# Kernel tuning notes

Measured on AMD Instinct MI355X. Metric: run time of the kernel, lower is better.

## Reference

```python
import jax, jax.numpy as jnp
import numpy as np

B, T, D = 4, 8192, 512
E, F, CAP = 8, 2048, 4096


def setup_inputs() -> dict:
    key = jax.random.key(0)
    ks = jax.random.split(key, 6)
    s = 0.02
    return {
        "x": jax.random.normal(ks[0], (B, T, D), dtype=jnp.float32),
        "Wr": jax.random.normal(ks[1], (D, E), dtype=jnp.float32) * s,
        "W1": jax.random.normal(ks[2], (E, D, F), dtype=jnp.float32) * s,
        "b1": jax.random.normal(ks[3], (E, F), dtype=jnp.float32) * s,
        "W2": jax.random.normal(ks[4], (E, F, D), dtype=jnp.float32) * s,
        "b2": jax.random.normal(ks[5], (E, D), dtype=jnp.float32) * s,
    }


def reference(x, Wr, W1, b1, W2, b2):
    Bb, Tt, Dd = x.shape
    N = Bb * Tt
    C = min(CAP, N)
    x_flat = x.reshape(N, Dd)
    logits = x_flat @ Wr                      # [N, E]
    probs = jax.nn.softmax(logits, axis=0)    # softmax over tokens (dim=0)
    # per-expert top-C tokens
    vals, idx = jax.lax.top_k(probs.T, C)     # [E, C]
    selected = x_flat[idx]                    # [E, C, D] gather
    h = jax.nn.gelu(jnp.einsum('ecd,edf->ecf', selected, W1) + b1[:, None, :],
                    approximate=False)
    out_e = jnp.einsum('ecf,efd->ecd', h, W2) + b2[:, None, :]  # [E, C, D]
    weighted = vals[..., None] * out_e
    output = jnp.zeros_like(x_flat).at[idx.reshape(-1)].add(weighted.reshape(-1, Dd))
    return output.reshape(Bb, Tt, Dd)
```

## Files before the change

kernel.cpp:

```cpp
#include <hip/hip_runtime.h>
#include <math.h>

#define N_TOK 32768
#define DIM 512
#define NE 8
#define NF 2048
#define CCAP 4096

typedef __attribute__((ext_vector_type(4))) float floatx4;
typedef __attribute__((ext_vector_type(8))) short shortx8;
typedef __attribute__((ext_vector_type(4))) short shortx4;

__device__ __forceinline__ short f2bf(float f) {
  union { float f; unsigned u; } v; v.f = f;
  unsigned r = v.u + 0x7FFFu + ((v.u >> 16) & 1u);
  return (short)(r >> 16);
}

__device__ __forceinline__ float bf2f(short s) {
  union { unsigned u; float f; } v; v.u = ((unsigned)(unsigned short)s) << 16;
  return v.f;
}

__device__ __forceinline__ unsigned f2key(float f) {
  union { float f; unsigned u; } v; v.f = f;
  return (v.u & 0x80000000u) ? ~v.u : (v.u | 0x80000000u);
}

__device__ __forceinline__ void gll16(const void* g, void* l) {
  __builtin_amdgcn_global_load_lds(
      (const __attribute__((address_space(1))) void*)g,
      (__attribute__((address_space(3))) void*)l, 16, 0, 0);
}

__device__ __forceinline__ float fast_gelu(float h) {
  float u = 0.7978845608f * (h + 0.044715f * h * h * h);
  float au = fabsf(u) * 2.885390082f;
  float z = __builtin_amdgcn_exp2f(au);
  float th = 1.0f - 2.0f * __builtin_amdgcn_rcpf(1.0f + z);
  th = copysignf(th, u);
  return 0.5f * h * (1.0f + th);
}

__device__ __forceinline__ void stage8_adv(const short** ap, short* dst, int t) {
#pragma unroll
  for (int i = 0; i < 8; i++) gll16(ap[i], dst + i * 2048 + t * 8);
#pragma unroll
  for (int i = 0; i < 8; i++) ap[i] += 64;
}

__device__ __forceinline__ void stage8_g2(const short* gA, short* dst, int t, int kk) {
#pragma unroll
  for (int i = 0; i < 8; i++)
    gll16(gA + (size_t)i * 32 * NF + kk * 64, dst + i * 2048 + t * 8);
}

__device__ __forceinline__ void loadB(const short* gB, int koff, int ldb, shortx8* bf) {
#pragma unroll
  for (int g = 0; g < 2; g++)
#pragma unroll
    for (int j = 0; j < 4; j++)
      bf[g * 4 + j] = *(const shortx8*)(gB + (size_t)j * 16 * ldb + koff + g * 32);
}

__device__ __forceinline__ void compute64r(const short* ldsA, const shortx8* bf,
                                           floatx4 (*acc)[4], int arow, int lx, int q) {
#pragma unroll
  for (int g = 0; g < 2; g++) {
    const int pu = (((g << 2) | q) ^ lx) << 3;
#pragma unroll
    for (int i = 0; i < 8; i++) {
      shortx8 af = *(const shortx8*)&ldsA[(arow + i * 16) * 64 + pu];
#pragma unroll
      for (int j = 0; j < 4; j++)
        acc[i][j] = __builtin_amdgcn_mfma_f32_16x16x32_bf16(af, bf[g * 4 + j], acc[i][j], 0, 0, 0);
    }
  }
}

__device__ __forceinline__ void xcd_map(int& bx, int& by, int& zi) {
  int lid = blockIdx.x + gridDim.x * (blockIdx.y + gridDim.y * blockIdx.z);
  int k = 8 / (int)gridDim.z;
  int x = lid & 7, rem = lid >> 3;
  zi = x / k;
  int bxy = rem * k + (x % k);
  bx = bxy % (int)gridDim.x;
  by = bxy / (int)gridDim.x;
}

__global__ __launch_bounds__(256) void k_prep(
    const float* __restrict__ x, const float* __restrict__ W1,
    const float* __restrict__ W2, const float* __restrict__ Wr,
    float* __restrict__ out, short* __restrict__ xb,
    short* __restrict__ w1t, short* __restrict__ w2t,
    float* __restrict__ logitsT, int* __restrict__ cnt) {
  __shared__ float tl[64 * 68];
  const int b = blockIdx.x, t = threadIdx.x;
  if (b < 4096) {
    const float* in;
    short* o;
    int R, C, c0, r0;
    if (b < 2048) {
      int e = b >> 8, tlid = b & 255;
      in = W1 + (size_t)e * DIM * NF;
      o = w1t + (size_t)e * NF * DIM;
      R = DIM; C = NF;
      c0 = (tlid & 31) * 64; r0 = (tlid >> 5) * 64;
    } else {
      int bb = b - 2048;
      int e = bb >> 8, tlid = bb & 255;
      in = W2 + (size_t)e * NF * DIM;
      o = w2t + (size_t)e * DIM * NF;
      R = NF; C = DIM;
      c0 = (tlid & 7) * 64; r0 = (tlid >> 3) * 64;
    }
    const int r = t >> 4, cq = (t & 15) * 4;
#pragma unroll
    for (int ii = 0; ii < 4; ii++) {
      floatx4 v = *(const floatx4*)&in[(size_t)(r0 + r + 16 * ii) * C + c0 + cq];
      *(floatx4*)&tl[(r + 16 * ii) * 68 + cq] = v;
    }
    __syncthreads();
    const int cc = t >> 2, rq = (t & 3) * 16;
    shortx8 o0, o1;
#pragma unroll
    for (int k = 0; k < 8; k++) o0[k] = f2bf(tl[(rq + k) * 68 + cc]);
#pragma unroll
    for (int k = 0; k < 8; k++) o1[k] = f2bf(tl[(rq + 8 + k) * 68 + cc]);
    size_t ob = (size_t)(c0 + cc) * R + r0 + rq;
    *(shortx8*)&o[ob] = o0;
    *(shortx8*)&o[ob + 8] = o1;
  } else if (b < 4608) {
    const int base = (b - 4096) * 8192 + t;
    floatx4 z = {0.f, 0.f, 0.f, 0.f};
#pragma unroll
    for (int i = 0; i < 32; i++) *(floatx4*)&out[(size_t)(base + i * 256) * 4] = z;
  } else if (b < 5120) {
    const int base = (b - 4608) * 8192 + t;
#pragma unroll
    for (int i = 0; i < 32; i++) {
      floatx4 v = *(const floatx4*)&x[(size_t)(base + i * 256) * 4];
      shortx4 s;
      s.x = f2bf(v.x); s.y = f2bf(v.y); s.z = f2bf(v.z); s.w = f2bf(v.w);
      *(shortx4*)&xb[(size_t)(base + i * 256) * 4] = s;
    }
  } else if (b < 6144) {
    const int lane = t & 63;
    const int wave = (b - 5120) * 4 + (t >> 6);
    float wr[64];
#pragma unroll
    for (int i = 0; i < 16; i++)
      *(floatx4*)&wr[i * 4] = *(const floatx4*)&Wr[lane * 64 + i * 4];
    for (int n = wave; n < N_TOK; n += 4096) {
      const float* xr = x + (size_t)n * DIM + lane * 8;
      floatx4 x0 = *(const floatx4*)xr;
      floatx4 x1 = *(const floatx4*)(xr + 4);
      float xs[8] = {x0.x, x0.y, x0.z, x0.w, x1.x, x1.y, x1.z, x1.w};
      double acc[8];
#pragma unroll
      for (int e2 = 0; e2 < 8; e2++) acc[e2] = 0.0;
#pragma unroll
      for (int j = 0; j < 8; j++) {
        double xv = (double)xs[j];
#pragma unroll
        for (int e2 = 0; e2 < 8; e2++) acc[e2] += xv * (double)wr[j * 8 + e2];
      }
#pragma unroll
      for (int e2 = 0; e2 < 8; e2++) {
#pragma unroll
        for (int off2 = 32; off2 > 0; off2 >>= 1)
          acc[e2] += __shfl_xor(acc[e2], off2);
      }
      double rv = acc[0];
#pragma unroll
      for (int e2 = 1; e2 < 8; e2++)
        if (lane == e2) rv = acc[e2];
      if (lane < 8) logitsT[(size_t)lane * N_TOK + n] = (float)rv;
    }
  } else {
#pragma unroll
    for (int i = 0; i < 128; i++) cnt[t + 256 * i] = 0;
  }
}

__global__ __launch_bounds__(1024) void k_select(const float* __restrict__ logitsT,
                                                 int* __restrict__ sel_idx,
                                                 float* __restrict__ sel_val,
                                                 int* __restrict__ cnt,
                                                 int* __restrict__ slots) {
  __shared__ float redf[16];
  __shared__ unsigned redu[16];
  __shared__ float s_max, s_inv;
  __shared__ unsigned s_tot;
  __shared__ unsigned s_cnt[2];
  const int e = blockIdx.x, t = threadIdx.x;
  const int wid = t >> 6, lane = t & 63;
  const float* lg = logitsT + (size_t)e * N_TOK;
  float lv[32];
  unsigned kv[32];
#pragma unroll
  for (int i = 0; i < 32; i++) lv[i] = lg[i * 1024 + t];
#pragma unroll
  for (int i = 0; i < 32; i++) kv[i] = f2key(lv[i]);
  float m = lv[0];
#pragma unroll
  for (int i = 1; i < 32; i++) m = fmaxf(m, lv[i]);
#pragma unroll
  for (int o = 32; o > 0; o >>= 1) m = fmaxf(m, __shfl_xor(m, o));
  if (lane == 0) redf[wid] = m;
  __syncthreads();
  if (t == 0) {
    float v = redf[0];
    for (int i = 1; i < 16; i++) v = fmaxf(v, redf[i]);
    s_max = v;
  }
  __syncthreads();
  m = s_max;
  float s = 0.f;
#pragma unroll
  for (int i = 0; i < 32; i++) s += expf(lv[i] - m);
#pragma unroll
  for (int o = 32; o > 0; o >>= 1) s += __shfl_xor(s, o);
  if (lane == 0) redf[wid] = s;
  __syncthreads();
  if (t == 0) {
    float v = 0.f;
    for (int i = 0; i < 16; i++) v += redf[i];
    s_inv = 1.0f / v;
  }
  unsigned T = 0;
  for (int bb = 31; bb >= 0; --bb) {
    unsigned cand = T | (1u << bb);
    unsigned c = 0;
#pragma unroll
    for (int i = 0; i < 32; i++) c += (kv[i] >= cand) ? 1u : 0u;
#pragma unroll
    for (int o = 32; o > 0; o >>= 1) c += __shfl_xor(c, o);
    if (lane == 0) redu[wid] = c;
    __syncthreads();
    if (t == 0) {
      unsigned v = 0;
      for (int i = 0; i < 16; i++) v += redu[i];
      s_tot = v;
    }
    __syncthreads();
    if (s_tot >= CCAP) T = cand;
  }
  {
    unsigned c = 0;
#pragma unroll
    for (int i = 0; i < 32; i++) c += (kv[i] > T) ? 1u : 0u;
#pragma unroll
    for (int o = 32; o > 0; o >>= 1) c += __shfl_xor(c, o);
    if (lane == 0) redu[wid] = c;
    __syncthreads();
    if (t == 0) {
      unsigned v = 0;
      for (int i = 0; i < 16; i++) v += redu[i];
      s_tot = v;
      s_cnt[0] = 0;
      s_cnt[1] = 0;
    }
    __syncthreads();
  }
  const unsigned rr = CCAP - s_tot;
  const float inv = s_inv;
  const unsigned long long lmask = (1ull << lane) - 1ull;
#pragma unroll
  for (int i = 0; i < 32; i++) {
    int n = i * 1024 + t;
    bool gt = kv[i] > T;
    bool eq = kv[i] == T;
    unsigned long long mg = __ballot(gt);
    unsigned long long mq = __ballot(eq);
    unsigned bg = 0, bq = 0;
    if (lane == 0) {
      if (mg) bg = atomicAdd(&s_cnt[0], (unsigned)__popcll(mg));
      if (mq) bq = atomicAdd(&s_cnt[1], (unsigned)__popcll(mq));
    }
    bg = __shfl(bg, 0);
    bq = __shfl(bq, 0);
    int pos = -1;
    if (gt) {
      pos = (int)(bg + (unsigned)__popcll(mg & lmask));
    } else if (eq) {
      unsigned qq = bq + (unsigned)__popcll(mq & lmask);
      if (qq < rr) pos = (int)(CCAP - rr + qq);
    }
    if (pos >= 0) {
      sel_idx[e * CCAP + pos] = n;
      sel_val[e * CCAP + pos] = expf(lv[i] - m) * inv;
      int s2 = atomicAdd(&cnt[n], 1);
      slots[n * 8 + s2] = (e << 16) | pos;
    }
  }
}

__global__ __launch_bounds__(256, 2) void k_gemm1(
    const short* __restrict__ xb, const short* __restrict__ w1t,
    const float* __restrict__ b1, const int* __restrict__ sel_idx,
    short* __restrict__ H, int e0) {
  __shared__ char smem[256 * 136 * 2];
  short* ldsA0 = (short*)smem;
  short* ldsA1 = (short*)(smem + 32768);

  int bx, by, zi;
  xcd_map(bx, by, zi);
  const int e = e0 + zi;
  const int c0 = by * 256;
  const int f0 = bx * 128;
  const int t = threadIdx.x;
  const int lane = t & 63;
  const int w = t >> 6;
  const int wm = w & 1, wn = w >> 1;
  const int row8 = t >> 3;
  const int su = (t & 7) ^ (row8 & 7);

  const short* gAp[8];
#pragma unroll
  for (int i = 0; i < 8; i++) {
    int tok = sel_idx[e * CCAP + c0 + row8 + i * 32];
    gAp[i] = xb + (size_t)tok * DIM + su * 8;
  }
  const short* gB = w1t + ((size_t)(e * NF + f0 + wn * 64 + (lane & 15))) * DIM + (lane >> 4) * 8;

  floatx4 acc[8][4];
#pragma unroll
  for (int i = 0; i < 8; i++)
#pragma unroll
    for (int j = 0; j < 4; j++) acc[i][j] = (floatx4){0.f, 0.f, 0.f, 0.f};

  const int arow = wm * 128 + (lane & 15);
  const int lx = lane & 7, q = lane >> 4;

  stage8_adv(gAp, ldsA0, t);
  __syncthreads();

  for (int kk = 0; kk < DIM / 64; kk += 2) {
    {
      shortx8 bf[8];
      loadB(gB, kk * 64, DIM, bf);
      __builtin_amdgcn_sched_barrier(0);
      stage8_adv(gAp, ldsA1, t);
      __builtin_amdgcn_sched_barrier(0);
      compute64r(ldsA0, bf, acc, arow, lx, q);
      __syncthreads();
    }
    {
      shortx8 bf[8];
      loadB(gB, (kk + 1) * 64, DIM, bf);
      __builtin_amdgcn_sched_barrier(0);
      if (kk + 2 < DIM / 64) stage8_adv(gAp, ldsA0, t);
      __builtin_amdgcn_sched_barrier(0);
      compute64r(ldsA1, bf, acc, arow, lx, q);
      __syncthreads();
    }
  }

  short* ep = (short*)smem;
  const int colL = wn * 64 + (lane & 15);
  const int rowL = wm * 128 + ((lane >> 4) << 2);
#pragma unroll
  for (int j = 0; j < 4; j++) {
    float bv = b1[e * NF + f0 + colL + j * 16];
#pragma unroll
    for (int i = 0; i < 8; i++) {
#pragma unroll
      for (int r = 0; r < 4; r++) {
        float h = acc[i][j][r] + bv;
        ep[(rowL + i * 16 + r) * 136 + colL + j * 16] = f2bf(fast_gelu(h));
      }
    }
  }
  __syncthreads();
  short* Hp = H + (size_t)zi * CCAP * NF;
  const int chunk = t & 15;
#pragma unroll
  for (int it = 0; it < 16; it++) {
    int r = (t >> 4) + 16 * it;
    shortx8 v = *(const shortx8*)&ep[r * 136 + chunk * 8];
    *(shortx8*)&Hp[(size_t)(c0 + r) * NF + f0 + chunk * 8] = v;
  }
}

__global__ __launch_bounds__(256, 2) void k_gemm2(
    const short* __restrict__ H, const short* __restrict__ w2t,
    const float* __restrict__ b2, short* __restrict__ oute, int e0) {
  __shared__ char smem[256 * 136 * 2];
  short* ldsA0 = (short*)smem;
  short* ldsA1 = (short*)(smem + 32768);

  int bx, by, zi;
  xcd_map(bx, by, zi);
  const int e = e0 + zi;
  const int c0 = by * 256;
  const int d0 = bx * 128;
  const int t = threadIdx.x;
  const int lane = t & 63;
  const int w = t >> 6;
  const int wm = w & 1, wn = w >> 1;
  const int row8 = t >> 3;
  const int su = (t & 7) ^ (row8 & 7);

  const short* gA = H + ((size_t)zi * CCAP + c0 + row8) * NF + su * 8;
  const short* gB = w2t + ((size_t)(e * DIM + d0 + wn * 64 + (lane & 15))) * NF + (lane >> 4) * 8;

  floatx4 acc[8][4];
#pragma unroll
  for (int i = 0; i < 8; i++)
#pragma unroll
    for (int j = 0; j < 4; j++) acc[i][j] = (floatx4){0.f, 0.f, 0.f, 0.f};

  const int arow = wm * 128 + (lane & 15);
  const int lx = lane & 7, q = lane >> 4;

  stage8_g2(gA, ldsA0, t, 0);
  __syncthreads();

  for (int kk = 0; kk < NF / 64; kk += 2) {
    {
      shortx8 bf[8];
      loadB(gB, kk * 64, NF, bf);
      __builtin_amdgcn_sched_barrier(0);
      stage8_g2(gA, ldsA1, t, kk + 1);
      __builtin_amdgcn_sched_barrier(0);
      compute64r(ldsA0, bf, acc, arow, lx, q);
      __syncthreads();
    }
    {
      shortx8 bf[8];
      loadB(gB, (kk + 1) * 64, NF, bf);
      __builtin_amdgcn_sched_barrier(0);
      if (kk + 2 < NF / 64) stage8_g2(gA, ldsA0, t, kk + 2);
      __builtin_amdgcn_sched_barrier(0);
      compute64r(ldsA1, bf, acc, arow, lx, q);
      __syncthreads();
    }
  }

  short* ep = (short*)smem;
  const int colL = wn * 64 + (lane & 15);
  const int rowL = wm * 128 + ((lane >> 4) << 2);
#pragma unroll
  for (int j = 0; j < 4; j++) {
    float bv = b2[e * DIM + d0 + colL + j * 16];
#pragma unroll
    for (int i = 0; i < 8; i++) {
#pragma unroll
      for (int r = 0; r < 4; r++) {
        float o = acc[i][j][r] + bv;
        ep[(rowL + i * 16 + r) * 136 + colL + j * 16] = f2bf(o);
      }
    }
  }
  __syncthreads();
  const int chunk = t & 15;
#pragma unroll
  for (int it = 0; it < 16; it++) {
    int r = (t >> 4) + 16 * it;
    shortx8 v = *(const shortx8*)&ep[r * 136 + chunk * 8];
    *(shortx8*)&oute[((size_t)e * CCAP + c0 + r) * DIM + d0 + chunk * 8] = v;
  }
}

__global__ __launch_bounds__(256) void k_combine(
    const short* __restrict__ oute, const int* __restrict__ cnt,
    const int* __restrict__ slots, const float* __restrict__ sel_val,
    float* __restrict__ out) {
  const int lane = threadIdx.x & 63;
  const int wid = threadIdx.x >> 6;
  const int n = blockIdx.x * 4 + wid;
  const int c = cnt[n];
  if (c == 0) return;
  float acc[8];
#pragma unroll
  for (int k = 0; k < 8; k++) acc[k] = 0.f;
  for (int s = 0; s < c; ++s) {
    int sl = slots[n * 8 + s];
    int e = sl >> 16, pos = sl & 0xFFFF;
    float val = sel_val[e * CCAP + pos];
    shortx8 v = *(const shortx8*)&oute[((size_t)e * CCAP + pos) * DIM + lane * 8];
#pragma unroll
    for (int k = 0; k < 8; k++) acc[k] += val * bf2f(v[k]);
  }
  floatx4 o0 = {acc[0], acc[1], acc[2], acc[3]};
  floatx4 o1 = {acc[4], acc[5], acc[6], acc[7]};
  *(floatx4*)&out[(size_t)n * DIM + lane * 8] = o0;
  *(floatx4*)&out[(size_t)n * DIM + lane * 8 + 4] = o1;
}

extern "C" void kernel_launch(void* const* d_in, const int* in_sizes, int n_in,
                              void* d_out, int out_size, void* d_ws, size_t ws_size,
                              hipStream_t stream) {
  const float* x = (const float*)d_in[0];
  const float* Wr = (const float*)d_in[1];
  const float* W1 = (const float*)d_in[2];
  const float* b1 = (const float*)d_in[3];
  const float* W2 = (const float*)d_in[4];
  const float* b2 = (const float*)d_in[5];
  float* out = (float*)d_out;

  char* p = (char*)d_ws;
  size_t off = 0;
  auto carve = [&](size_t bytes) {
    void* r = p + off;
    off = (off + bytes + 255) & ~(size_t)255;
    return r;
  };
  short* xb = (short*)carve((size_t)N_TOK * DIM * 2);
  short* w1t = (short*)carve((size_t)NE * NF * DIM * 2);
  short* w2t = (short*)carve((size_t)NE * DIM * NF * 2);
  float* logitsT = (float*)carve((size_t)NE * N_TOK * 4);
  int* selidx = (int*)carve((size_t)NE * CCAP * 4);
  float* selval = (float*)carve((size_t)NE * CCAP * 4);
  int* cnt = (int*)carve((size_t)N_TOK * 4);
  int* slots = (int*)carve((size_t)N_TOK * 8 * 4);
  short* oute = (short*)carve((size_t)NE * CCAP * DIM * 2);
  const size_t hbytes = (size_t)CCAP * NF * 2;
  int g = 1;
  if (off + 8 * hbytes <= ws_size) g = 8;
  else if (off + 4 * hbytes <= ws_size) g = 4;
  else if (off + 2 * hbytes <= ws_size) g = 2;
  short* Hbuf = (short*)carve((size_t)g * hbytes);

  k_prep<<<6145, 256, 0, stream>>>(x, W1, W2, Wr, out, xb, w1t, w2t, logitsT, cnt);
  k_select<<<NE, 1024, 0, stream>>>(logitsT, selidx, selval, cnt, slots);
  for (int e0 = 0; e0 < NE; e0 += g) {
    k_gemm1<<<dim3(NF / 128, CCAP / 256, g), 256, 0, stream>>>(xb, w1t, b1, selidx, Hbuf, e0);
    k_gemm2<<<dim3(DIM / 128, CCAP / 256, g), 256, 0, stream>>>(Hbuf, w2t, b2, oute, e0);
  }
  k_combine<<<N_TOK / 4, 256, 0, stream>>>(oute, cnt, slots, selval, out);
}
```

Baseline: 525.8 us.

## Halve GEMM M-tile to 128 rows and drop separate output zeroing

Both expert GEMMs go from 256x128 to 128x128 tiles with half the LDS and accumulators. Launch bounds rise to 4 blocks per SM and the grid doubles, aiming at more occupancy and better wave balance, especially for gemm2 with its small N. The epilogue now writes through LDS in two 64-row chunks with extra barriers. The zero-fill of out in prep is removed and combine writes zeros for tokens no expert picked, saving one full pass over the output.

```diff
diff --git a/kernel.cpp b/kernel.cpp
--- a/kernel.cpp
+++ b/kernel.cpp
@@ -42,16 +42,16 @@
   return 0.5f * h * (1.0f + th);
 }
 
-__device__ __forceinline__ void stage8_adv(const short** ap, short* dst, int t) {
-#pragma unroll
-  for (int i = 0; i < 8; i++) gll16(ap[i], dst + i * 2048 + t * 8);
-#pragma unroll
-  for (int i = 0; i < 8; i++) ap[i] += 64;
-}
-
-__device__ __forceinline__ void stage8_g2(const short* gA, short* dst, int t, int kk) {
-#pragma unroll
-  for (int i = 0; i < 8; i++)
+__device__ __forceinline__ void stage4_adv(const short** ap, short* dst, int t) {
+#pragma unroll
+  for (int i = 0; i < 4; i++) gll16(ap[i], dst + i * 2048 + t * 8);
+#pragma unroll
+  for (int i = 0; i < 4; i++) ap[i] += 64;
+}
+
+__device__ __forceinline__ void stage4_g2(const short* gA, short* dst, int t, int kk) {
+#pragma unroll
+  for (int i = 0; i < 4; i++)
     gll16(gA + (size_t)i * 32 * NF + kk * 64, dst + i * 2048 + t * 8);
 }
 
@@ -63,13 +63,13 @@
       bf[g * 4 + j] = *(const shortx8*)(gB + (size_t)j * 16 * ldb + koff + g * 32);
 }
 
-__device__ __forceinline__ void compute64r(const short* ldsA, const shortx8* bf,
+__device__ __forceinline__ void compute64w(const short* ldsA, const shortx8* bf,
                                            floatx4 (*acc)[4], int arow, int lx, int q) {
 #pragma unroll
   for (int g = 0; g < 2; g++) {
     const int pu = (((g << 2) | q) ^ lx) << 3;
 #pragma unroll
-    for (int i = 0; i < 8; i++) {
+    for (int i = 0; i < 4; i++) {
       shortx8 af = *(const shortx8*)&ldsA[(arow + i * 16) * 64 + pu];
 #pragma unroll
       for (int j = 0; j < 4; j++)
@@ -91,8 +91,7 @@
 __global__ __launch_bounds__(256) void k_prep(
     const float* __restrict__ x, const float* __restrict__ W1,
     const float* __restrict__ W2, const float* __restrict__ Wr,
-    float* __restrict__ out, short* __restrict__ xb,
-    short* __restrict__ w1t, short* __restrict__ w2t,
+    short* __restrict__ xb, short* __restrict__ w1t, short* __restrict__ w2t,
     float* __restrict__ logitsT, int* __restrict__ cnt) {
   __shared__ float tl[64 * 68];
   const int b = blockIdx.x, t = threadIdx.x;
@@ -132,11 +131,6 @@
     *(shortx8*)&o[ob + 8] = o1;
   } else if (b < 4608) {
     const int base = (b - 4096) * 8192 + t;
-    floatx4 z = {0.f, 0.f, 0.f, 0.f};
-#pragma unroll
-    for (int i = 0; i < 32; i++) *(floatx4*)&out[(size_t)(base + i * 256) * 4] = z;
-  } else if (b < 5120) {
-    const int base = (b - 4608) * 8192 + t;
 #pragma unroll
     for (int i = 0; i < 32; i++) {
       floatx4 v = *(const floatx4*)&x[(size_t)(base + i * 256) * 4];
@@ -144,9 +138,9 @@
       s.x = f2bf(v.x); s.y = f2bf(v.y); s.z = f2bf(v.z); s.w = f2bf(v.w);
       *(shortx4*)&xb[(size_t)(base + i * 256) * 4] = s;
     }
-  } else if (b < 6144) {
+  } else if (b < 5632) {
     const int lane = t & 63;
-    const int wave = (b - 5120) * 4 + (t >> 6);
+    const int wave = (b - 4608) * 4 + (t >> 6);
     float wr[64];
 #pragma unroll
     for (int i = 0; i < 16; i++)
@@ -296,18 +290,18 @@
   }
 }
 
-__global__ __launch_bounds__(256, 2) void k_gemm1(
+__global__ __launch_bounds__(256, 4) void k_gemm1(
     const short* __restrict__ xb, const short* __restrict__ w1t,
     const float* __restrict__ b1, const int* __restrict__ sel_idx,
     short* __restrict__ H, int e0) {
-  __shared__ char smem[256 * 136 * 2];
+  __shared__ char smem[32768];
   short* ldsA0 = (short*)smem;
-  short* ldsA1 = (short*)(smem + 32768);
+  short* ldsA1 = (short*)(smem + 16384);
 
   int bx, by, zi;
   xcd_map(bx, by, zi);
   const int e = e0 + zi;
-  const int c0 = by * 256;
+  const int c0 = by * 128;
   const int f0 = bx * 128;
   const int t = threadIdx.x;
   const int lane = t & 63;
@@ -316,24 +310,24 @@
   const int row8 = t >> 3;
   const int su = (t & 7) ^ (row8 & 7);
 
-  const short* gAp[8];
-#pragma unroll
-  for (int i = 0; i < 8; i++) {
-    int tok = sel_idx[e * CCAP + c0 + row8 + i * 32];
+  const short* gAp[4];
+#pragma unroll
+  for (int i = 0; i < 4; i++) {
+    int tok = sel_idx[e * CCAP + c0 + i * 32 + row8];
     gAp[i] = xb + (size_t)tok * DIM + su * 8;
   }
   const short* gB = w1t + ((size_t)(e * NF + f0 + wn * 64 + (lane & 15))) * DIM + (lane >> 4) * 8;
 
-  floatx4 acc[8][4];
-#pragma unroll
-  for (int i = 0; i < 8; i++)
+  floatx4 acc[4][4];
+#pragma unroll
+  for (int i = 0; i < 4; i++)
 #pragma unroll
     for (int j = 0; j < 4; j++) acc[i][j] = (floatx4){0.f, 0.f, 0.f, 0.f};
 
-  const int arow = wm * 128 + (lane & 15);
+  const int arow = wm * 64 + (lane & 15);
   const int lx = lane & 7, q = lane >> 4;
 
-  stage8_adv(gAp, ldsA0, t);
+  stage4_adv(gAp, ldsA0, t);
   __syncthreads();
 
   for (int kk = 0; kk < DIM / 64; kk += 2) {
@@ -341,59 +335,65 @@
       shortx8 bf[8];
       loadB(gB, kk * 64, DIM, bf);
       __builtin_amdgcn_sched_barrier(0);
-      stage8_adv(gAp, ldsA1, t);
-      __builtin_amdgcn_sched_barrier(0);
-      compute64r(ldsA0, bf, acc, arow, lx, q);
+      stage4_adv(gAp, ldsA1, t);
+      __builtin_amdgcn_sched_barrier(0);
+      compute64w(ldsA0, bf, acc, arow, lx, q);
       __syncthreads();
     }
     {
       shortx8 bf[8];
       loadB(gB, (kk + 1) * 64, DIM, bf);
       __builtin_amdgcn_sched_barrier(0);
-      if (kk + 2 < DIM / 64) stage8_adv(gAp, ldsA0, t);
-      __builtin_amdgcn_sched_barrier(0);
-      compute64r(ldsA1, bf, acc, arow, lx, q);
+      if (kk + 2 < DIM / 64) stage4_adv(gAp, ldsA0, t);
+      __builtin_amdgcn_sched_barrier(0);
+      compute64w(ldsA1, bf, acc, arow, lx, q);
       __syncthreads();
     }
   }
 
   short* ep = (short*)smem;
   const int colL = wn * 64 + (lane & 15);
-  const int rowL = wm * 128 + ((lane >> 4) << 2);
-#pragma unroll
-  for (int j = 0; j < 4; j++) {
-    float bv = b1[e * NF + f0 + colL + j * 16];
-#pragma unroll
-    for (int i = 0; i < 8; i++) {
-#pragma unroll
-      for (int r = 0; r < 4; r++) {
-        float h = acc[i][j][r] + bv;
-        ep[(rowL + i * 16 + r) * 136 + colL + j * 16] = f2bf(fast_gelu(h));
+  const int rowL = (lane >> 4) << 2;
+  short* Hp = H + (size_t)zi * CCAP * NF;
+#pragma unroll
+  for (int ch = 0; ch < 2; ch++) {
+    if (wm == ch) {
+#pragma unroll
+      for (int j = 0; j < 4; j++) {
+        float bv = b1[e * NF + f0 + colL + j * 16];
+#pragma unroll
+        for (int i = 0; i < 4; i++) {
+#pragma unroll
+          for (int r = 0; r < 4; r++) {
+            float h = acc[i][j][r] + bv;
+            ep[(i * 16 + rowL + r) * 136 + colL + j * 16] = f2bf(fast_gelu(h));
+          }
+        }
       }
     }
-  }
-  __syncthreads();
-  short* Hp = H + (size_t)zi * CCAP * NF;
-  const int chunk = t & 15;
-#pragma unroll
-  for (int it = 0; it < 16; it++) {
-    int r = (t >> 4) + 16 * it;
-    shortx8 v = *(const shortx8*)&ep[r * 136 + chunk * 8];
-    *(shortx8*)&Hp[(size_t)(c0 + r) * NF + f0 + chunk * 8] = v;
-  }
-}
-
-__global__ __launch_bounds__(256, 2) void k_gemm2(
+    __syncthreads();
+    const int chunk = t & 15;
+#pragma unroll
+    for (int it = 0; it < 4; it++) {
+      int r = (t >> 4) + 16 * it;
+      shortx8 v = *(const shortx8*)&ep[r * 136 + chunk * 8];
+      *(shortx8*)&Hp[(size_t)(c0 + ch * 64 + r) * NF + f0 + chunk * 8] = v;
+    }
+    __syncthreads();
+  }
+}
+
+__global__ __launch_bounds__(256, 4) void k_gemm2(
     const short* __restrict__ H, const short* __restrict__ w2t,
     const float* __restrict__ b2, short* __restrict__ oute, int e0) {
-  __shared__ char smem[256 * 136 * 2];
+  __shared__ char smem[32768];
   short* ldsA0 = (short*)smem;
-  short* ldsA1 = (short*)(smem + 32768);
+  short* ldsA1 = (short*)(smem + 16384);
 
   int bx, by, zi;
   xcd_map(bx, by, zi);
   const int e = e0 + zi;
-  const int c0 = by * 256;
+  const int c0 = by * 128;
   const int d0 = bx * 128;
   const int t = threadIdx.x;
   const int lane = t & 63;
@@ -405,16 +405,16 @@
   const short* gA = H + ((size_t)zi * CCAP + c0 + row8) * NF + su * 8;
   const short* gB = w2t + ((size_t)(e * DIM + d0 + wn * 64 + (lane & 15))) * NF + (lane >> 4) * 8;
 
-  floatx4 acc[8][4];
-#pragma unroll
-  for (int i = 0; i < 8; i++)
+  floatx4 acc[4][4];
+#pragma unroll
+  for (int i = 0; i < 4; i++)
 #pragma unroll
     for (int j = 0; j < 4; j++) acc[i][j] = (floatx4){0.f, 0.f, 0.f, 0.f};
 
-  const int arow = wm * 128 + (lane & 15);
+  const int arow = wm * 64 + (lane & 15);
   const int lx = lane & 7, q = lane >> 4;
 
-  stage8_g2(gA, ldsA0, t, 0);
+  stage4_g2(gA, ldsA0, t, 0);
   __syncthreads();
 
   for (int kk = 0; kk < NF / 64; kk += 2) {
@@ -422,44 +422,50 @@
       shortx8 bf[8];
       loadB(gB, kk * 64, NF, bf);
       __builtin_amdgcn_sched_barrier(0);
-      stage8_g2(gA, ldsA1, t, kk + 1);
-      __builtin_amdgcn_sched_barrier(0);
-      compute64r(ldsA0, bf, acc, arow, lx, q);
+      stage4_g2(gA, ldsA1, t, kk + 1);
+      __builtin_amdgcn_sched_barrier(0);
+      compute64w(ldsA0, bf, acc, arow, lx, q);
       __syncthreads();
     }
     {
       shortx8 bf[8];
       loadB(gB, (kk + 1) * 64, NF, bf);
       __builtin_amdgcn_sched_barrier(0);
-      if (kk + 2 < NF / 64) stage8_g2(gA, ldsA0, t, kk + 2);
-      __builtin_amdgcn_sched_barrier(0);
-      compute64r(ldsA1, bf, acc, arow, lx, q);
+      if (kk + 2 < NF / 64) stage4_g2(gA, ldsA0, t, kk + 2);
+      __builtin_amdgcn_sched_barrier(0);
+      compute64w(ldsA1, bf, acc, arow, lx, q);
       __syncthreads();
     }
   }
 
   short* ep = (short*)smem;
   const int colL = wn * 64 + (lane & 15);
-  const int rowL = wm * 128 + ((lane >> 4) << 2);
-#pragma unroll
-  for (int j = 0; j < 4; j++) {
-    float bv = b2[e * DIM + d0 + colL + j * 16];
-#pragma unroll
-    for (int i = 0; i < 8; i++) {
-#pragma unroll
-      for (int r = 0; r < 4; r++) {
-        float o = acc[i][j][r] + bv;
-        ep[(rowL + i * 16 + r) * 136 + colL + j * 16] = f2bf(o);
+  const int rowL = (lane >> 4) << 2;
+#pragma unroll
+  for (int ch = 0; ch < 2; ch++) {
+    if (wm == ch) {
+#pragma unroll
+      for (int j = 0; j < 4; j++) {
+        float bv = b2[e * DIM + d0 + colL + j * 16];
+#pragma unroll
+        for (int i = 0; i < 4; i++) {
+#pragma unroll
+          for (int r = 0; r < 4; r++) {
+            float o = acc[i][j][r] + bv;
+            ep[(i * 16 + rowL + r) * 136 + colL + j * 16] = f2bf(o);
+          }
+        }
       }
     }
-  }
-  __syncthreads();
-  const int chunk = t & 15;
-#pragma unroll
-  for (int it = 0; it < 16; it++) {
-    int r = (t >> 4) + 16 * it;
-    shortx8 v = *(const shortx8*)&ep[r * 136 + chunk * 8];
-    *(shortx8*)&oute[((size_t)e * CCAP + c0 + r) * DIM + d0 + chunk * 8] = v;
+    __syncthreads();
+    const int chunk = t & 15;
+#pragma unroll
+    for (int it = 0; it < 4; it++) {
+      int r = (t >> 4) + 16 * it;
+      shortx8 v = *(const shortx8*)&ep[r * 136 + chunk * 8];
+      *(shortx8*)&oute[((size_t)e * CCAP + c0 + ch * 64 + r) * DIM + d0 + chunk * 8] = v;
+    }
+    __syncthreads();
   }
 }
 
@@ -471,7 +477,6 @@
   const int wid = threadIdx.x >> 6;
   const int n = blockIdx.x * 4 + wid;
   const int c = cnt[n];
-  if (c == 0) return;
   float acc[8];
 #pragma unroll
   for (int k = 0; k < 8; k++) acc[k] = 0.f;
@@ -523,11 +528,11 @@
   else if (off + 2 * hbytes <= ws_size) g = 2;
   short* Hbuf = (short*)carve((size_t)g * hbytes);
 
-  k_prep<<<6145, 256, 0, stream>>>(x, W1, W2, Wr, out, xb, w1t, w2t, logitsT, cnt);
+  k_prep<<<5633, 256, 0, stream>>>(x, W1, W2, Wr, xb, w1t, w2t, logitsT, cnt);
   k_select<<<NE, 1024, 0, stream>>>(logitsT, selidx, selval, cnt, slots);
   for (int e0 = 0; e0 < NE; e0 += g) {
-    k_gemm1<<<dim3(NF / 128, CCAP / 256, g), 256, 0, stream>>>(xb, w1t, b1, selidx, Hbuf, e0);
-    k_gemm2<<<dim3(DIM / 128, CCAP / 256, g), 256, 0, stream>>>(Hbuf, w2t, b2, oute, e0);
+    k_gemm1<<<dim3(NF / 128, CCAP / 128, g), 256, 0, stream>>>(xb, w1t, b1, selidx, Hbuf, e0);
+    k_gemm2<<<dim3(DIM / 128, CCAP / 128, g), 256, 0, stream>>>(Hbuf, w2t, b2, oute, e0);
   }
   k_combine<<<N_TOK / 4, 256, 0, stream>>>(oute, cnt, slots, selval, out);
 }
```

Result: slower. 615.4 us (+17.0%).

## Split B-fragment loads into half-K prefetch and fuse prep passes

Applied to the files above, without the earlier changes.

Both expert GEMMs now load the B fragments for each 64-wide K step in two 32-wide halves. The next half is prefetched into registers while MFMAs run on the current half, using a single-step loop with swapped LDS buffers instead of a two-way unrolled loop. This is meant to hide global-load latency with fewer live registers. The prep kernel also folds the x-to-bf16 conversion into the router-logit pass so x is read once, and it drops the separate zeroing of the output. The combine kernel now writes zeros for tokens that no expert selected, which adds writes for those tokens.

```diff
diff --git a/kernel.cpp b/kernel.cpp
--- a/kernel.cpp
+++ b/kernel.cpp
@@ -42,39 +42,23 @@
   return 0.5f * h * (1.0f + th);
 }
 
-__device__ __forceinline__ void stage8_adv(const short** ap, short* dst, int t) {
-#pragma unroll
-  for (int i = 0; i < 8; i++) gll16(ap[i], dst + i * 2048 + t * 8);
-#pragma unroll
-  for (int i = 0; i < 8; i++) ap[i] += 64;
-}
-
-__device__ __forceinline__ void stage8_g2(const short* gA, short* dst, int t, int kk) {
-#pragma unroll
-  for (int i = 0; i < 8; i++)
-    gll16(gA + (size_t)i * 32 * NF + kk * 64, dst + i * 2048 + t * 8);
-}
-
-__device__ __forceinline__ void loadB(const short* gB, int koff, int ldb, shortx8* bf) {
-#pragma unroll
-  for (int g = 0; g < 2; g++)
+#define SB __builtin_amdgcn_sched_barrier(0)
+
+__device__ __forceinline__ void loadBg(const short* gB, int kk, int g, int ldb, shortx8* bf) {
+#pragma unroll
+  for (int j = 0; j < 4; j++)
+    bf[j] = *(const shortx8*)(gB + (size_t)j * 16 * ldb + kk * 64 + g * 32);
+}
+
+__device__ __forceinline__ void computeHalf(const short* ldsA, const shortx8* bf,
+                                            floatx4 (*acc)[4], int arow, int lx, int q, int g) {
+  const int pu = (((g << 2) | q) ^ lx) << 3;
+#pragma unroll
+  for (int i = 0; i < 8; i++) {
+    shortx8 af = *(const shortx8*)&ldsA[(arow + i * 16) * 64 + pu];
 #pragma unroll
     for (int j = 0; j < 4; j++)
-      bf[g * 4 + j] = *(const shortx8*)(gB + (size_t)j * 16 * ldb + koff + g * 32);
-}
-
-__device__ __forceinline__ void compute64r(const short* ldsA, const shortx8* bf,
-                                           floatx4 (*acc)[4], int arow, int lx, int q) {
-#pragma unroll
-  for (int g = 0; g < 2; g++) {
-    const int pu = (((g << 2) | q) ^ lx) << 3;
-#pragma unroll
-    for (int i = 0; i < 8; i++) {
-      shortx8 af = *(const shortx8*)&ldsA[(arow + i * 16) * 64 + pu];
-#pragma unroll
-      for (int j = 0; j < 4; j++)
-        acc[i][j] = __builtin_amdgcn_mfma_f32_16x16x32_bf16(af, bf[g * 4 + j], acc[i][j], 0, 0, 0);
-    }
+      acc[i][j] = __builtin_amdgcn_mfma_f32_16x16x32_bf16(af, bf[j], acc[i][j], 0, 0, 0);
   }
 }
 
@@ -91,8 +75,7 @@
 __global__ __launch_bounds__(256) void k_prep(
     const float* __restrict__ x, const float* __restrict__ W1,
     const float* __restrict__ W2, const float* __restrict__ Wr,
-    float* __restrict__ out, short* __restrict__ xb,
-    short* __restrict__ w1t, short* __restrict__ w2t,
+    short* __restrict__ xb, short* __restrict__ w1t, short* __restrict__ w2t,
     float* __restrict__ logitsT, int* __restrict__ cnt) {
   __shared__ float tl[64 * 68];
   const int b = blockIdx.x, t = threadIdx.x;
@@ -130,23 +113,9 @@
     size_t ob = (size_t)(c0 + cc) * R + r0 + rq;
     *(shortx8*)&o[ob] = o0;
     *(shortx8*)&o[ob + 8] = o1;
-  } else if (b < 4608) {
-    const int base = (b - 4096) * 8192 + t;
-    floatx4 z = {0.f, 0.f, 0.f, 0.f};
-#pragma unroll
-    for (int i = 0; i < 32; i++) *(floatx4*)&out[(size_t)(base + i * 256) * 4] = z;
   } else if (b < 5120) {
-    const int base = (b - 4608) * 8192 + t;
-#pragma unroll
-    for (int i = 0; i < 32; i++) {
-      floatx4 v = *(const floatx4*)&x[(size_t)(base + i * 256) * 4];
-      shortx4 s;
-      s.x = f2bf(v.x); s.y = f2bf(v.y); s.z = f2bf(v.z); s.w = f2bf(v.w);
-      *(shortx4*)&xb[(size_t)(base + i * 256) * 4] = s;
-    }
-  } else if (b < 6144) {
     const int lane = t & 63;
-    const int wave = (b - 5120) * 4 + (t >> 6);
+    const int wave = (b - 4096) * 4 + (t >> 6);
     float wr[64];
 #pragma unroll
     for (int i = 0; i < 16; i++)
@@ -156,6 +125,10 @@
       floatx4 x0 = *(const floatx4*)xr;
       floatx4 x1 = *(const floatx4*)(xr + 4);
       float xs[8] = {x0.x, x0.y, x0.z, x0.w, x1.x, x1.y, x1.z, x1.w};
+      shortx8 sv;
+#pragma unroll
+      for (int j = 0; j < 8; j++) sv[j] = f2bf(xs[j]);
+      *(shortx8*)&xb[(size_t)n * DIM + lane * 8] = sv;
       double acc[8];
 #pragma unroll
       for (int e2 = 0; e2 < 8; e2++) acc[e2] = 0.0;
@@ -301,8 +274,8 @@
     const float* __restrict__ b1, const int* __restrict__ sel_idx,
     short* __restrict__ H, int e0) {
   __shared__ char smem[256 * 136 * 2];
-  short* ldsA0 = (short*)smem;
-  short* ldsA1 = (short*)(smem + 32768);
+  short* l0 = (short*)smem;
+  short* l1 = (short*)(smem + 32768);
 
   int bx, by, zi;
   xcd_map(bx, by, zi);
@@ -316,11 +289,11 @@
   const int row8 = t >> 3;
   const int su = (t & 7) ^ (row8 & 7);
 
-  const short* gAp[8];
+  unsigned offA[8];
 #pragma unroll
   for (int i = 0; i < 8; i++) {
     int tok = sel_idx[e * CCAP + c0 + row8 + i * 32];
-    gAp[i] = xb + (size_t)tok * DIM + su * 8;
+    offA[i] = (unsigned)tok * DIM + su * 8;
   }
   const short* gB = w1t + ((size_t)(e * NF + f0 + wn * 64 + (lane & 15))) * DIM + (lane >> 4) * 8;
 
@@ -333,28 +306,31 @@
   const int arow = wm * 128 + (lane & 15);
   const int lx = lane & 7, q = lane >> 4;
 
-  stage8_adv(gAp, ldsA0, t);
-  __syncthreads();
-
-  for (int kk = 0; kk < DIM / 64; kk += 2) {
-    {
-      shortx8 bf[8];
-      loadB(gB, kk * 64, DIM, bf);
-      __builtin_amdgcn_sched_barrier(0);
-      stage8_adv(gAp, ldsA1, t);
-      __builtin_amdgcn_sched_barrier(0);
-      compute64r(ldsA0, bf, acc, arow, lx, q);
-      __syncthreads();
-    }
-    {
-      shortx8 bf[8];
-      loadB(gB, (kk + 1) * 64, DIM, bf);
-      __builtin_amdgcn_sched_barrier(0);
-      if (kk + 2 < DIM / 64) stage8_adv(gAp, ldsA0, t);
-      __builtin_amdgcn_sched_barrier(0);
-      compute64r(ldsA1, bf, acc, arow, lx, q);
-      __syncthreads();
-    }
+  shortx8 bfE[4], bfO[4];
+  loadBg(gB, 0, 0, DIM, bfE);
+  SB;
+#pragma unroll
+  for (int i = 0; i < 8; i++) gll16(xb + offA[i], l0 + i * 2048 + t * 8);
+  __syncthreads();
+
+  short *cur = l0, *nxt = l1;
+  const int NK = DIM / 64;
+  for (int kk = 0; kk < NK; ++kk) {
+    loadBg(gB, kk, 1, DIM, bfO);
+    SB;
+    if (kk + 1 < NK) {
+#pragma unroll
+      for (int i = 0; i < 8; i++)
+        gll16(xb + offA[i] + (kk + 1) * 64, nxt + i * 2048 + t * 8);
+    }
+    SB;
+    computeHalf(cur, bfE, acc, arow, lx, q, 0);
+    SB;
+    if (kk + 1 < NK) loadBg(gB, kk + 1, 0, DIM, bfE);
+    SB;
+    computeHalf(cur, bfO, acc, arow, lx, q, 1);
+    __syncthreads();
+    short* tmp = cur; cur = nxt; nxt = tmp;
   }
 
   short* ep = (short*)smem;
@@ -387,8 +363,8 @@
     const short* __restrict__ H, const short* __restrict__ w2t,
     const float* __restrict__ b2, short* __restrict__ oute, int e0) {
   __shared__ char smem[256 * 136 * 2];
-  short* ldsA0 = (short*)smem;
-  short* ldsA1 = (short*)(smem + 32768);
+  short* l0 = (short*)smem;
+  short* l1 = (short*)(smem + 32768);
 
   int bx, by, zi;
   xcd_map(bx, by, zi);
@@ -414,28 +390,32 @@
   const int arow = wm * 128 + (lane & 15);
   const int lx = lane & 7, q = lane >> 4;
 
-  stage8_g2(gA, ldsA0, t, 0);
-  __syncthreads();
-
-  for (int kk = 0; kk < NF / 64; kk += 2) {
-    {
-      shortx8 bf[8];
-      loadB(gB, kk * 64, NF, bf);
-      __builtin_amdgcn_sched_barrier(0);
-      stage8_g2(gA, ldsA1, t, kk + 1);
-      __builtin_amdgcn_sched_barrier(0);
-      compute64r(ldsA0, bf, acc, arow, lx, q);
-      __syncthreads();
-    }
-    {
-      shortx8 bf[8];
-      loadB(gB, (kk + 1) * 64, NF, bf);
-      __builtin_amdgcn_sched_barrier(0);
-      if (kk + 2 < NF / 64) stage8_g2(gA, ldsA0, t, kk + 2);
-      __builtin_amdgcn_sched_barrier(0);
-      compute64r(ldsA1, bf, acc, arow, lx, q);
-      __syncthreads();
-    }
+  shortx8 bfE[4], bfO[4];
+  loadBg(gB, 0, 0, NF, bfE);
+  SB;
+#pragma unroll
+  for (int i = 0; i < 8; i++)
+    gll16(gA + (size_t)i * 32 * NF, l0 + i * 2048 + t * 8);
+  __syncthreads();
+
+  short *cur = l0, *nxt = l1;
+  const int NK = NF / 64;
+  for (int kk = 0; kk < NK; ++kk) {
+    loadBg(gB, kk, 1, NF, bfO);
+    SB;
+    if (kk + 1 < NK) {
+#pragma unroll
+      for (int i = 0; i < 8; i++)
+        gll16(gA + (size_t)i * 32 * NF + (kk + 1) * 64, nxt + i * 2048 + t * 8);
+    }
+    SB;
+    computeHalf(cur, bfE, acc, arow, lx, q, 0);
+    SB;
+    if (kk + 1 < NK) loadBg(gB, kk + 1, 0, NF, bfE);
+    SB;
+    computeHalf(cur, bfO, acc, arow, lx, q, 1);
+    __syncthreads();
+    short* tmp = cur; cur = nxt; nxt = tmp;
   }
 
   short* ep = (short*)smem;
@@ -471,7 +451,6 @@
   const int wid = threadIdx.x >> 6;
   const int n = blockIdx.x * 4 + wid;
   const int c = cnt[n];
-  if (c == 0) return;
   float acc[8];
 #pragma unroll
   for (int k = 0; k < 8; k++) acc[k] = 0.f;
@@ -523,7 +502,7 @@
   else if (off + 2 * hbytes <= ws_size) g = 2;
   short* Hbuf = (short*)carve((size_t)g * hbytes);
 
-  k_prep<<<6145, 256, 0, stream>>>(x, W1, W2, Wr, out, xb, w1t, w2t, logitsT, cnt);
+  k_prep<<<5121, 256, 0, stream>>>(x, W1, W2, Wr, xb, w1t, w2t, logitsT, cnt);
   k_select<<<NE, 1024, 0, stream>>>(logitsT, selidx, selval, cnt, slots);
   for (int e0 = 0; e0 < NE; e0 += g) {
     k_gemm1<<<dim3(NF / 128, CCAP / 256, g), 256, 0, stream>>>(xb, w1t, b1, selidx, Hbuf, e0);
```

After: 477.6 us. -9.2%, faster.
